# Performance work log

Measured on AMD Instinct MI355X. Metric: run time of the kernel, lower is better.

Reference implementation:

```python
import jax, jax.numpy as jnp
import numpy as np

MARGIN = 5.0
NUM_CLASSES = 21


def setup_inputs() -> dict:
    key = jax.random.key(0)
    k1, k2, k3 = jax.random.split(key, 3)
    B, D, C = 65536, 512, NUM_CLASSES
    features = jax.random.normal(k1, (B, D), dtype=jnp.float32)
    centers = jax.random.normal(k2, (C, D), dtype=jnp.float32)
    labels = jax.random.randint(k3, (B,), 0, C, dtype=jnp.int64)
    return {"features": features, "centers": centers, "labels": labels}


def reference(features, centers, labels):
    # Halved squared euclidean distances, batch x num_classes, via the
    # ||f||^2 + ||c||^2 - 2 f.c expansion (avoids a B x C x D intermediate).
    f2 = jnp.sum(features * features, axis=1, keepdims=True)      # (B, 1)
    c2 = jnp.sum(centers * centers, axis=1)[None, :]              # (1, C)
    d = 0.5 * (f2 + c2 - 2.0 * (features @ centers.T))            # (B, C)

    B = features.shape[0]
    pos = d[jnp.arange(B), labels]                                 # dist to own center
    same = labels[:, None] == jnp.arange(NUM_CLASSES)[None, :]     # (B, C)
    neg = jnp.min(jnp.where(same, jnp.inf, d), axis=1)             # nearest other center
    loss = jnp.mean(jax.nn.relu(pos + MARGIN - neg))
    return loss
```

## Files before the change

### kernel.cpp

```cpp
#include <hip/hip_runtime.h>
#include <float.h>

#define DIM      512
#define NCLS     21
#define MARGIN_V 5.0f
#define ROWS_PB  64
#define DC       32
#define NSTAGE   (DIM / DC)
#define LPAD     (DC + 1)

__global__ __launch_bounds__(64)
void center_norm_kernel(const float* __restrict__ centers,
                        float* __restrict__ halfc2) {
    const int c = blockIdx.x;
    const int t = threadIdx.x;
    float s = 0.f;
#pragma unroll
    for (int i = 0; i < DIM / 64; ++i) {
        float v = centers[c * DIM + i * 64 + t];
        s = fmaf(v, v, s);
    }
#pragma unroll
    for (int off = 32; off > 0; off >>= 1)
        s += __shfl_down(s, off, 64);
    if (t == 0) halfc2[c] = 0.5f * s;
}

__global__ __launch_bounds__(64)
void tcl_main_kernel(const float* __restrict__ feat,
                     const float* __restrict__ centers,
                     const int* __restrict__ labels,
                     const float* __restrict__ halfc2,
                     float* __restrict__ out) {
    __shared__ float tile[ROWS_PB * LPAD];
    const int t    = threadIdx.x;
    const int row0 = blockIdx.x * ROWS_PB;

    const int lab = labels[row0 + t];

    float acc[NCLS];
#pragma unroll
    for (int c = 0; c < NCLS; ++c) acc[c] = 0.f;

    const float4* fbase = reinterpret_cast<const float4*>(feat);

    float4 pre[8];
#pragma unroll
    for (int i = 0; i < 8; ++i) {
        int f = i * 64 + t;
        int row = f >> 3, j4 = f & 7;
        pre[i] = fbase[(size_t)(row0 + row) * (DIM / 4) + j4];
    }

#pragma unroll 1
    for (int s = 0; s < NSTAGE; ++s) {
        __syncthreads();
#pragma unroll
        for (int i = 0; i < 8; ++i) {
            int f = i * 64 + t;
            int row = f >> 3, j4 = f & 7;
            int base = row * LPAD + j4 * 4;
            tile[base + 0] = pre[i].x;
            tile[base + 1] = pre[i].y;
            tile[base + 2] = pre[i].z;
            tile[base + 3] = pre[i].w;
        }
        __syncthreads();
        if (s + 1 < NSTAGE) {
#pragma unroll
            for (int i = 0; i < 8; ++i) {
                int f = i * 64 + t;
                int row = f >> 3, j4 = f & 7;
                pre[i] = fbase[(size_t)(row0 + row) * (DIM / 4)
                               + (size_t)(s + 1) * (DC / 4) + j4];
            }
        }
        const int dbase = s * DC;
#pragma unroll 2
        for (int jj = 0; jj < DC; jj += 4) {
            float f0 = tile[t * LPAD + jj + 0];
            float f1 = tile[t * LPAD + jj + 1];
            float f2 = tile[t * LPAD + jj + 2];
            float f3 = tile[t * LPAD + jj + 3];
#pragma unroll
            for (int c = 0; c < NCLS; ++c) {
                const float* cp = &centers[c * DIM + dbase + jj];
                acc[c] = fmaf(f0, cp[0],
                          fmaf(f1, cp[1],
                           fmaf(f2, cp[2],
                            fmaf(f3, cp[3], acc[c]))));
            }
        }
    }

    float pos = 0.f, neg = FLT_MAX;
#pragma unroll
    for (int c = 0; c < NCLS; ++c) {
        float e = halfc2[c] - acc[c];
        pos = (c == lab) ? e : pos;
        neg = (c == lab) ? neg : fminf(neg, e);
    }
    float v = fmaxf(pos + MARGIN_V - neg, 0.f);

#pragma unroll
    for (int off = 32; off > 0; off >>= 1)
        v += __shfl_down(v, off, 64);
    if (t == 0) atomicAdd(out, v * (1.0f / 65536.f));
}

extern "C" void kernel_launch(void* const* d_in, const int* in_sizes, int n_in,
                              void* d_out, int out_size, void* d_ws, size_t ws_size,
                              hipStream_t stream) {
    const float* feat    = (const float*)d_in[0];
    const float* centers = (const float*)d_in[1];
    const int*   labels  = (const int*)d_in[2];
    float* out    = (float*)d_out;
    float* halfc2 = (float*)d_ws;

    hipMemsetAsync(d_out, 0, (size_t)out_size * sizeof(float), stream);
    center_norm_kernel<<<NCLS, 64, 0, stream>>>(centers, halfc2);

    const int nblocks = 65536 / ROWS_PB;
    tcl_main_kernel<<<nblocks, 64, 0, stream>>>(feat, centers, labels, halfc2, out);
}
```

Before: 254.0 us.

## Split feature dimension across four waves per block with XOR-swizzled LDS tiles

Each 64-row block now uses four wavefronts, and each wave handles a quarter of the 512-wide feature dimension. Partial dot products are combined through shared memory before wave 0 computes the loss. Each wave stages its own slice in an XOR-swizzled LDS tile, which allows float4 reads without padding or block-wide barriers in the main loop. The register prefetch double-buffering is dropped in favour of more waves per CU to hide latency. The cost is a shared-memory reduction and a larger LDS footprint.

Result: slower. 416.5 us (+64.0%).

```diff
diff --git a/kernel.cpp b/kernel.cpp
--- a/kernel.cpp
+++ b/kernel.cpp
@@ -5,9 +5,11 @@
 #define NCLS     21
 #define MARGIN_V 5.0f
 #define ROWS_PB  64
+#define NWAVES   4
+#define WSLICE   (DIM / NWAVES)
 #define DC       32
-#define NSTAGE   (DIM / DC)
-#define LPAD     (DC + 1)
+#define NSTAGE   (WSLICE / DC)
+#define REDS     23
 
 __global__ __launch_bounds__(64)
 void center_norm_kernel(const float* __restrict__ centers,
@@ -26,86 +28,85 @@
     if (t == 0) halfc2[c] = 0.5f * s;
 }
 
-__global__ __launch_bounds__(64)
+__global__ __launch_bounds__(256, 4)
 void tcl_main_kernel(const float* __restrict__ feat,
                      const float* __restrict__ centers,
                      const int* __restrict__ labels,
                      const float* __restrict__ halfc2,
                      float* __restrict__ out) {
-    __shared__ float tile[ROWS_PB * LPAD];
-    const int t    = threadIdx.x;
+    __shared__ float smem[NWAVES * ROWS_PB * DC];
+
+    const int tid  = threadIdx.x;
+    const int w    = tid >> 6;
+    const int t    = tid & 63;
     const int row0 = blockIdx.x * ROWS_PB;
 
-    const int lab = labels[row0 + t];
+    float4* tile4 = reinterpret_cast<float4*>(smem + w * (ROWS_PB * DC));
+
+    const float4* fb = reinterpret_cast<const float4*>(feat)
+                     + (size_t)row0 * (DIM / 4) + w * (WSLICE / 4);
 
     float acc[NCLS];
 #pragma unroll
     for (int c = 0; c < NCLS; ++c) acc[c] = 0.f;
 
-    const float4* fbase = reinterpret_cast<const float4*>(feat);
-
-    float4 pre[8];
-#pragma unroll
-    for (int i = 0; i < 8; ++i) {
-        int f = i * 64 + t;
-        int row = f >> 3, j4 = f & 7;
-        pre[i] = fbase[(size_t)(row0 + row) * (DIM / 4) + j4];
-    }
+    const int xr = t & 7;
 
 #pragma unroll 1
     for (int s = 0; s < NSTAGE; ++s) {
-        __syncthreads();
+        float4 v[8];
 #pragma unroll
-        for (int i = 0; i < 8; ++i) {
-            int f = i * 64 + t;
-            int row = f >> 3, j4 = f & 7;
-            int base = row * LPAD + j4 * 4;
-            tile[base + 0] = pre[i].x;
-            tile[base + 1] = pre[i].y;
-            tile[base + 2] = pre[i].z;
-            tile[base + 3] = pre[i].w;
+        for (int k = 0; k < 8; ++k) {
+            int slot = k * 64 + t;
+            int r    = slot >> 3;
+            int j4   = (slot & 7) ^ (r & 7);
+            v[k] = fb[(size_t)r * (DIM / 4) + s * (DC / 4) + j4];
         }
-        __syncthreads();
-        if (s + 1 < NSTAGE) {
 #pragma unroll
-            for (int i = 0; i < 8; ++i) {
-                int f = i * 64 + t;
-                int row = f >> 3, j4 = f & 7;
-                pre[i] = fbase[(size_t)(row0 + row) * (DIM / 4)
-                               + (size_t)(s + 1) * (DC / 4) + j4];
-            }
-        }
-        const int dbase = s * DC;
-#pragma unroll 2
-        for (int jj = 0; jj < DC; jj += 4) {
-            float f0 = tile[t * LPAD + jj + 0];
-            float f1 = tile[t * LPAD + jj + 1];
-            float f2 = tile[t * LPAD + jj + 2];
-            float f3 = tile[t * LPAD + jj + 3];
+        for (int k = 0; k < 8; ++k)
+            tile4[k * 64 + t] = v[k];
+
+        const int dbase = w * WSLICE + s * DC;
+#pragma unroll
+        for (int jj4 = 0; jj4 < 8; ++jj4) {
+            float4 f = tile4[t * 8 + (jj4 ^ xr)];
+            const int d = dbase + jj4 * 4;
 #pragma unroll
             for (int c = 0; c < NCLS; ++c) {
-                const float* cp = &centers[c * DIM + dbase + jj];
-                acc[c] = fmaf(f0, cp[0],
-                          fmaf(f1, cp[1],
-                           fmaf(f2, cp[2],
-                            fmaf(f3, cp[3], acc[c]))));
+                const float* cp = &centers[c * DIM + d];
+                acc[c] = fmaf(f.x, cp[0],
+                          fmaf(f.y, cp[1],
+                           fmaf(f.z, cp[2],
+                            fmaf(f.w, cp[3], acc[c]))));
             }
         }
     }
 
-    float pos = 0.f, neg = FLT_MAX;
+    __syncthreads();
 #pragma unroll
-    for (int c = 0; c < NCLS; ++c) {
-        float e = halfc2[c] - acc[c];
-        pos = (c == lab) ? e : pos;
-        neg = (c == lab) ? neg : fminf(neg, e);
+    for (int c = 0; c < NCLS; ++c)
+        smem[(w * ROWS_PB + t) * REDS + c] = acc[c];
+    __syncthreads();
+
+    if (w == 0) {
+        const int lab = labels[row0 + t];
+        float pos = 0.f, neg = FLT_MAX;
+#pragma unroll
+        for (int c = 0; c < NCLS; ++c) {
+            float dot = smem[(0 * ROWS_PB + t) * REDS + c]
+                      + smem[(1 * ROWS_PB + t) * REDS + c]
+                      + smem[(2 * ROWS_PB + t) * REDS + c]
+                      + smem[(3 * ROWS_PB + t) * REDS + c];
+            float e = halfc2[c] - dot;
+            pos = (c == lab) ? e : pos;
+            neg = (c == lab) ? neg : fminf(neg, e);
+        }
+        float vv = fmaxf(pos + MARGIN_V - neg, 0.f);
+#pragma unroll
+        for (int off = 32; off > 0; off >>= 1)
+            vv += __shfl_down(vv, off, 64);
+        if (t == 0) atomicAdd(out, vv * (1.0f / 65536.f));
     }
-    float v = fmaxf(pos + MARGIN_V - neg, 0.f);
-
-#pragma unroll
-    for (int off = 32; off > 0; off >>= 1)
-        v += __shfl_down(v, off, 64);
-    if (t == 0) atomicAdd(out, v * (1.0f / 65536.f));
 }
 
 extern "C" void kernel_launch(void* const* d_in, const int* in_sizes, int n_in,
@@ -121,5 +122,5 @@
     center_norm_kernel<<<NCLS, 64, 0, stream>>>(centers, halfc2);
 
     const int nblocks = 65536 / ROWS_PB;
-    tcl_main_kernel<<<nblocks, 64, 0, stream>>>(feat, centers, labels, halfc2, out);
+    tcl_main_kernel<<<nblocks, 256, 0, stream>>>(feat, centers, labels, halfc2, out);
 }
```
